# Kernel optimization log

Measured on AMD Instinct MI355X. Metric: run time of the kernel, lower is better.

## Reference

```python
import jax, jax.numpy as jnp
import numpy as np

K = 4          # conv kernel size
DIL = 3        # conv dilation
EPS = 1e-5     # rms eps inside gate kernel
NORM_EPS = 1e-5  # RMSNorm eps for value rms


def setup_inputs() -> dict:
    key = jax.random.key(0)
    ks = jax.random.split(key, 10)
    B, T, G, C, E = 2, 4096, 4, 1024, 1024
    return {
        "embeddings": jax.random.normal(ks[0], (B, T, E), jnp.float32),
        "hidden_states": jax.random.normal(ks[1], (B, T, G, C), jnp.float32),
        "key_w": jax.random.normal(ks[2], (G * C, E), jnp.float32) * 0.02,
        "key_b": jax.random.normal(ks[3], (G * C,), jnp.float32) * 0.02,
        "value_w": jax.random.normal(ks[4], (C, E), jnp.float32) * 0.02,
        "value_b": jax.random.normal(ks[5], (C,), jnp.float32) * 0.02,
        "w_key_norm": jax.random.uniform(ks[6], (G, C), jnp.float32, 0.5, 1.5),
        "w_query_norm": jax.random.uniform(ks[7], (G, C), jnp.float32, 0.5, 1.5),
        "w_norm": jax.random.uniform(ks[8], (G, C), jnp.float32, 0.5, 1.5),
        "conv_weight": jax.random.normal(ks[9], (G * C, K), jnp.float32) * 0.1,
    }


def reference(embeddings, hidden_states, key_w, key_b, value_w, value_b,
              w_key_norm, w_query_norm, w_norm, conv_weight):
    B, T, G, C = hidden_states.shape
    # projections
    k_all = (embeddings @ key_w.T + key_b).reshape(B, T, G, C)     # [B,T,G,C]
    q_all = hidden_states                                          # [B,T,G,C]
    vproj = embeddings @ value_w.T + value_b                       # [B,T,C]

    # gate kernel: per (b,t,g) RMS of key/query + weighted dot -> sign-sqrt-sigmoid gate
    rms_k = jnp.sqrt(jnp.mean(k_all * k_all, axis=-1) + EPS)       # [B,T,G]
    rms_q = jnp.sqrt(jnp.mean(q_all * q_all, axis=-1) + EPS)       # [B,T,G]
    dot = jnp.einsum('btgc,gc,btgc,gc->btg', k_all, w_key_norm, q_all, w_query_norm)
    gate_raw = dot / (rms_k * rms_q) / jnp.sqrt(jnp.float32(C))
    gate = jax.nn.sigmoid(jnp.where(gate_raw >= 0, 1.0, -1.0)
                          * jnp.sqrt(jnp.maximum(jnp.abs(gate_raw), 1e-6)))
    value = vproj[:, :, None, :] * gate[..., None]                 # [B,T,G,C]
    rms_v = jnp.sqrt(jnp.mean(value * value, axis=-1) + NORM_EPS)  # [B,T,G]

    # conv+residual kernel: per-group RMS-norm, dilated depthwise causal conv, SiLU, residual
    normed = value * (w_norm[None, None] / rms_v[..., None])       # [B,T,G,C]
    conv_w = conv_weight.reshape(G, C, K)                          # depthwise weights
    pad = (K - 1) * DIL
    xp = jnp.pad(normed, ((0, 0), (pad, 0), (0, 0), (0, 0)))
    # acc[b,t,g,c] = sum_k normed[b, t-(K-1-k)*DIL, g, c] * conv_w[g,c,k]
    acc = xp[:, 0:T] * conv_w[None, None, :, :, 0]
    for k in range(1, K):
        acc = acc + xp[:, k * DIL: k * DIL + T] * conv_w[None, None, :, :, k]
    acc = acc * jax.nn.sigmoid(acc)  # SiLU activation
    return value + acc
```

## Files before the change

### kernel.cpp

```cpp
#include <hip/hip_runtime.h>
#include <hip/hip_bf16.h>
#include <cstdint>
#include <cstddef>

using bf16 = __hip_bfloat16;

typedef __bf16 bf16x8_t __attribute__((ext_vector_type(8)));
typedef float  f32x4_t  __attribute__((ext_vector_type(4)));

static constexpr int Bb = 2;
static constexpr int Tt = 4096;
static constexpr int Gg = 4;
static constexpr int Cc = 1024;
static constexpr int Mm = Bb * Tt;
static constexpr int GC = Gg * Cc;

__device__ __forceinline__ float bfbits2f(unsigned u) {
  union { unsigned i; float f; } c; c.i = u << 16; return c.f;
}
__device__ __forceinline__ ushort f2bfbits(float v) {
  union { __hip_bfloat16 h; ushort u; } c; c.h = __float2bfloat16(v); return c.u;
}

__device__ __forceinline__ void store_val(bf16* p, float v)  { *p = __float2bfloat16(v); }
__device__ __forceinline__ void store_val(float* p, float v) { *p = v; }

__device__ __forceinline__ void gld_lds16(const ushort* g, ushort* l) {
  __builtin_amdgcn_global_load_lds(
      (const __attribute__((address_space(1))) void*)g,
      (__attribute__((address_space(3))) void*)l, 16, 0, 0);
}

__global__ __launch_bounds__(256)
void cvt_bf16(const float* __restrict__ in, ushort* __restrict__ out, int n4)
{
  const int i = blockIdx.x * 256 + threadIdx.x;
  if (i >= n4) return;
  const float4 v = ((const float4*)in)[i];
  ushort4 o;
  o.x = f2bfbits(v.x); o.y = f2bfbits(v.y);
  o.z = f2bfbits(v.z); o.w = f2bfbits(v.w);
  ((ushort4*)out)[i] = o;
}

__global__ __launch_bounds__(256)
void cvt_split(const float* __restrict__ in, ushort* __restrict__ hi,
               ushort* __restrict__ lo, int n4)
{
  const int i = blockIdx.x * 256 + threadIdx.x;
  if (i >= n4) return;
  const float4 v = ((const float4*)in)[i];
  ushort4 h, l;
  h.x = f2bfbits(v.x); l.x = f2bfbits(v.x - bfbits2f(h.x));
  h.y = f2bfbits(v.y); l.y = f2bfbits(v.y - bfbits2f(h.y));
  h.z = f2bfbits(v.z); l.z = f2bfbits(v.z - bfbits2f(h.z));
  h.w = f2bfbits(v.w); l.w = f2bfbits(v.w - bfbits2f(h.w));
  ((ushort4*)hi)[i] = h;
  ((ushort4*)lo)[i] = l;
}

__global__ __launch_bounds__(512, 1)
void gemm_key_fused(const ushort* __restrict__ embH, const ushort* __restrict__ embL,
                    const ushort* __restrict__ kwH,  const ushort* __restrict__ kwL,
                    const float* __restrict__ key_b, const float* __restrict__ hid,
                    const float* __restrict__ wkn,   const float* __restrict__ wqn,
                    float* __restrict__ k2_part, float* __restrict__ dot_part,
                    float* __restrict__ q2_part)
{
  constexpr int NT = 32;
  __shared__ __align__(16) ushort sA[2 * 16384];
  __shared__ __align__(16) ushort sB[2 * 16384];

  const int tid  = threadIdx.x;
  const int lane = tid & 63;
  const int wave = tid >> 6;
  const int wm   = wave & 1;
  const int wn   = wave >> 1;
  const int l15  = lane & 15;
  const int cHk  = (lane >> 4) ^ (lane & 7);
  const int row0 = blockIdx.y * 256;
  const int col0 = blockIdx.x * 256;

  const int sRow = tid >> 3;
  const int schk = (tid & 7) ^ (sRow & 7);
  const ushort* aSel = (schk < 4) ? embH : embL;
  const ushort* bSel = (schk < 4) ? kwH  : kwL;
  const int sel8 = (schk & 3) * 8;
  const int wofs = wave * 512;

  auto stageA = [&](int rb, int u, int b) {
    const size_t co = (size_t)u * 32 + sel8;
    gld_lds16(aSel + (size_t)(row0 + rb + sRow) * Cc + co,
              sA + b * 16384 + (rb >> 6) * 4096 + wofs);
    gld_lds16(aSel + (size_t)(row0 + rb + 64 + sRow) * Cc + co,
              sA + b * 16384 + ((rb >> 6) + 1) * 4096 + wofs);
  };
  auto stageB = [&](int rb, int u, int b) {
    const size_t co = (size_t)u * 32 + sel8;
    gld_lds16(bSel + (size_t)(col0 + rb + sRow) * Cc + co,
              sB + b * 16384 + (rb >> 6) * 4096 + wofs);
    gld_lds16(bSel + (size_t)(col0 + rb + 64 + sRow) * Cc + co,
              sB + b * 16384 + ((rb >> 6) + 1) * 4096 + wofs);
  };

  f32x4_t acc[2][2][4][2] = {};

#define MFMA3(QM, QN, AH, AL, BH, BL)                                       \
  _Pragma("unroll") for (int mi = 0; mi < 4; ++mi)                          \
    _Pragma("unroll") for (int ni = 0; ni < 2; ++ni) {                      \
      acc[QM][QN][mi][ni] = __builtin_amdgcn_mfma_f32_16x16x32_bf16(        \
          AH[mi], BH[ni], acc[QM][QN][mi][ni], 0, 0, 0);                    \
      acc[QM][QN][mi][ni] = __builtin_amdgcn_mfma_f32_16x16x32_bf16(        \
          AH[mi], BL[ni], acc[QM][QN][mi][ni], 0, 0, 0);                    \
      acc[QM][QN][mi][ni] = __builtin_amdgcn_mfma_f32_16x16x32_bf16(        \
          AL[mi], BH[ni], acc[QM][QN][mi][ni], 0, 0, 0);                    \
    }

  stageA(0, 0, 0); stageB(0, 0, 0); stageB(128, 0, 0); stageA(128, 0, 0);
  asm volatile("s_waitcnt vmcnt(0)" ::: "memory");
  __builtin_amdgcn_s_barrier();

  for (int u = 0; u < NT; ++u) {
    const int b = u & 1, nb = b ^ 1;
    const ushort* bufA = sA + b * 16384;
    const ushort* bufB = sB + b * 16384;
    if (u + 1 < NT) {
      stageA(0, u + 1, nb);   stageB(0, u + 1, nb);
      stageB(128, u + 1, nb); stageA(128, u + 1, nb);
    }

    bf16x8_t b0H[2], b0L[2], b1H[2], b1L[2];
#pragma unroll
    for (int ni = 0; ni < 2; ++ni) {
      const ushort* p0 = bufB + (wn * 32 + ni * 16 + l15) * 64;
      const ushort* p1 = bufB + (128 + wn * 32 + ni * 16 + l15) * 64;
      b0H[ni] = *(const bf16x8_t*)(p0 + cHk * 8);
      b0L[ni] = *(const bf16x8_t*)(p0 + (cHk ^ 4) * 8);
      b1H[ni] = *(const bf16x8_t*)(p1 + cHk * 8);
      b1L[ni] = *(const bf16x8_t*)(p1 + (cHk ^ 4) * 8);
    }
    bf16x8_t a0H[4], a0L[4];
#pragma unroll
    for (int mi = 0; mi < 4; ++mi) {
      const ushort* pa = bufA + (wm * 64 + mi * 16 + l15) * 64;
      a0H[mi] = *(const bf16x8_t*)(pa + cHk * 8);
      a0L[mi] = *(const bf16x8_t*)(pa + (cHk ^ 4) * 8);
    }
    __builtin_amdgcn_s_setprio(1);
    MFMA3(0, 0, a0H, a0L, b0H, b0L)
    __builtin_amdgcn_s_setprio(0);
    bf16x8_t a1H[4], a1L[4];
#pragma unroll
    for (int mi = 0; mi < 4; ++mi) {
      const ushort* pa = bufA + (128 + wm * 64 + mi * 16 + l15) * 64;
      a1H[mi] = *(const bf16x8_t*)(pa + cHk * 8);
      a1L[mi] = *(const bf16x8_t*)(pa + (cHk ^ 4) * 8);
    }
    __builtin_amdgcn_s_setprio(1);
    MFMA3(0, 1, a0H, a0L, b1H, b1L)
    MFMA3(1, 0, a1H, a1L, b0H, b0L)
    MFMA3(1, 1, a1H, a1L, b1H, b1L)
    __builtin_amdgcn_s_setprio(0);

    asm volatile("s_waitcnt lgkmcnt(0)" ::: "memory");
    asm volatile("s_waitcnt vmcnt(0)" ::: "memory");
    __builtin_amdgcn_s_barrier();
  }
#undef MFMA3

  const int lrow = lane >> 4;
  const int lcol = lane & 15;
  const int g    = col0 >> 10;

#pragma unroll
  for (int qm = 0; qm < 2; ++qm) {
    float s2[4][4] = {}, su[4][4] = {}, sq[4][4] = {};
#pragma unroll
    for (int qn = 0; qn < 2; ++qn)
#pragma unroll
      for (int ni = 0; ni < 2; ++ni) {
        const int col = col0 + qn * 128 + wn * 32 + ni * 16 + lcol;
        const float kb = key_b[col];
        const float ww = wkn[col] * wqn[col];
#pragma unroll
        for (int mi = 0; mi < 4; ++mi) {
          const int rowb = row0 + qm * 128 + wm * 64 + mi * 16 + lrow * 4;
#pragma unroll
          for (int r = 0; r < 4; ++r) {
            const float q = hid[(size_t)(rowb + r) * GC + col];
            const float k = acc[qm][qn][mi][ni][r] + kb;
            s2[mi][r] += k * k;
            su[mi][r] += k * ww * q;
            sq[mi][r] += q * q;
          }
        }
      }
#pragma unroll
    for (int off = 1; off < 16; off <<= 1) {
#pragma unroll
      for (int mi = 0; mi < 4; ++mi)
#pragma unroll
        for (int r = 0; r < 4; ++r) {
          s2[mi][r] += __shfl_xor(s2[mi][r], off);
          su[mi][r] += __shfl_xor(su[mi][r], off);
          sq[mi][r] += __shfl_xor(sq[mi][r], off);
        }
    }
    if (lcol == 0) {
#pragma unroll
      for (int mi = 0; mi < 4; ++mi) {
        const int rowb = row0 + qm * 128 + wm * 64 + mi * 16 + lrow * 4;
#pragma unroll
        for (int r = 0; r < 4; ++r) {
          atomicAdd(&k2_part[(rowb + r) * Gg + g],  s2[mi][r]);
          atomicAdd(&dot_part[(rowb + r) * Gg + g], su[mi][r]);
          atomicAdd(&q2_part[(rowb + r) * Gg + g],  sq[mi][r]);
        }
      }
    }
  }
}

template <typename OutT>
__global__ __launch_bounds__(256, 4)
void gemm_bt(const ushort* __restrict__ A, const ushort* __restrict__ Bm,
             const float* __restrict__ bias, OutT* __restrict__ C,
             int M, int N, int K)
{
  __shared__ __align__(16) ushort sA[128 * 64];
  __shared__ __align__(16) ushort sB[128 * 64];

  const int tid  = threadIdx.x;
  const int lane = tid & 63;
  const int wave = tid >> 6;
  const int wm   = wave & 1;
  const int wn   = wave >> 1;
  const int row0 = blockIdx.y * 128;
  const int col0 = blockIdx.x * 128;

  const int srow = tid >> 3;
  const int scol = ((tid & 7) ^ (srow & 7)) * 8;
  ushort* aWB = sA + wave * 512;
  ushort* bWB = sB + wave * 512;

  f32x4_t acc[4][4] = {};

  for (int kt = 0; kt < K; kt += 64) {
#pragma unroll
    for (int p = 0; p < 4; ++p) {
      gld_lds16(A  + (size_t)(row0 + p * 32 + srow) * K + kt + scol,
                aWB + p * 2048);
      gld_lds16(Bm + (size_t)(col0 + p * 32 + srow) * K + kt + scol,
                bWB + p * 2048);
    }
    __syncthreads();

#pragma unroll
    for (int ks = 0; ks < 2; ++ks) {
      const int cb = ks * 4 + (lane >> 4);
      const int ce = ((cb ^ (lane & 7)) * 8);
      bf16x8_t af[4], bfr[4];
#pragma unroll
      for (int mi = 0; mi < 4; ++mi) {
        const int r = wm * 64 + mi * 16 + (lane & 15);
        af[mi] = *(const bf16x8_t*)(sA + r * 64 + ce);
      }
#pragma unroll
      for (int ni = 0; ni < 4; ++ni) {
        const int r = wn * 64 + ni * 16 + (lane & 15);
        bfr[ni] = *(const bf16x8_t*)(sB + r * 64 + ce);
      }
#pragma unroll
      for (int mi = 0; mi < 4; ++mi)
#pragma unroll
        for (int ni = 0; ni < 4; ++ni)
          acc[mi][ni] = __builtin_amdgcn_mfma_f32_16x16x32_bf16(
              af[mi], bfr[ni], acc[mi][ni], 0, 0, 0);
    }
    __syncthreads();
  }

  const int lrow = lane >> 4;
  const int lcol = lane & 15;
#pragma unroll
  for (int ni = 0; ni < 4; ++ni) {
    const int col = col0 + wn * 64 + ni * 16 + lcol;
    const float bv = bias[col];
#pragma unroll
    for (int mi = 0; mi < 4; ++mi) {
      const int rowb = row0 + wm * 64 + mi * 16 + lrow * 4;
#pragma unroll
      for (int r = 0; r < 4; ++r)
        store_val(&C[(size_t)(rowb + r) * N + col], acc[mi][ni][r] + bv);
    }
  }
}

__global__ __launch_bounds__(256)
void finalize_kernel(const float* __restrict__ vproj,
                     const float* __restrict__ k2_part,
                     const float* __restrict__ dot_part,
                     const float* __restrict__ q2_part,
                     float* __restrict__ gate_o, float* __restrict__ snorm_o)
{
  const int bt   = blockIdx.x;
  const int tid  = threadIdx.x;
  const int g    = tid >> 6;
  const int lane = tid & 63;

  const float4 v4 = ((const float4*)(vproj + (size_t)bt * Cc))[tid];
  float pv = v4.x * v4.x + v4.y * v4.y + v4.z * v4.z + v4.w * v4.w;
#pragma unroll
  for (int off = 32; off > 0; off >>= 1) pv += __shfl_xor(pv, off);
  __shared__ float wsum[4];
  if (lane == 0) wsum[g] = pv;
  __syncthreads();

  if (lane == 0) {
    const float mv = (wsum[0] + wsum[1] + wsum[2] + wsum[3]) * (1.0f / 1024.0f);
    const float sk = k2_part[bt * Gg + g];
    const float sd = dot_part[bt * Gg + g];
    const float sq = q2_part[bt * Gg + g];
    const float rk = sqrtf(sk * (1.0f / 1024.0f) + 1e-5f);
    const float rq = sqrtf(sq * (1.0f / 1024.0f) + 1e-5f);
    const float graw = sd / (rk * rq) * (1.0f / 32.0f);
    const float sgn = (graw >= 0.f) ? 1.f : -1.f;
    const float gate = 1.f / (1.f + expf(-sgn * sqrtf(fmaxf(fabsf(graw), 1e-6f))));
    const float rv = sqrtf(gate * gate * mv + 1e-5f);
    gate_o[bt * Gg + g]  = gate;
    snorm_o[bt * Gg + g] = gate / rv;
  }
}

static constexpr int CJ  = 128;
static constexpr int NCH = 11;

__global__ __launch_bounds__(256)
void conv_kernel(const float* __restrict__ vproj, const float* __restrict__ gate,
                 const float* __restrict__ snorm, const float* __restrict__ wnm,
                 const float* __restrict__ cw, float* __restrict__ out)
{
  int x = blockIdx.x;
  const int cb = x & 3;  x >>= 2;
  const int p  = x % 3;  x /= 3;
  const int ch = x % NCH; x /= NCH;
  const int g  = x & 3;  x >>= 2;
  const int b  = x;
  const int c  = cb * 256 + threadIdx.x;

  const float wn = wnm[g * Cc + c];
  const float4 w = ((const float4*)cw)[g * Cc + c];

  int t = p + 3 * (ch * CJ);
  if (t >= Tt) return;

  float n1 = 0.f, n2 = 0.f, n3 = 0.f;
#pragma unroll
  for (int h = 3; h >= 1; --h) {
    const int th = t - 3 * h;
    float nv = 0.f;
    if (th >= 0) {
      const int bt = b * Tt + th;
      nv = vproj[(size_t)bt * Cc + c] * snorm[bt * Gg + g] * wn;
    }
    n3 = n2; n2 = n1; n1 = nv;
  }

  for (int j = 0; j < CJ && t < Tt; ++j, t += 3) {
    const int bt = b * Tt + t;
    const float vp  = vproj[(size_t)bt * Cc + c];
    const float gt  = gate[bt * Gg + g];
    const float sn  = snorm[bt * Gg + g];
    const float cur = vp * sn * wn;
    const float a   = w.x * n3 + w.y * n2 + w.z * n1 + w.w * cur;
    const float si  = a / (1.f + __expf(-a));
    out[((size_t)bt * Gg + g) * Cc + c] = vp * gt + si;
    n3 = n2; n2 = n1; n1 = cur;
  }
}

extern "C" void kernel_launch(void* const* d_in, const int* in_sizes, int n_in,
                              void* d_out, int out_size, void* d_ws, size_t ws_size,
                              hipStream_t stream)
{
  const float* emb   = (const float*)d_in[0];
  const float* hid   = (const float*)d_in[1];
  const float* key_w = (const float*)d_in[2];
  const float* key_b = (const float*)d_in[3];
  const float* val_w = (const float*)d_in[4];
  const float* val_b = (const float*)d_in[5];
  const float* wkn   = (const float*)d_in[6];
  const float* wqn   = (const float*)d_in[7];
  const float* wnm   = (const float*)d_in[8];
  const float* cwt   = (const float*)d_in[9];
  float* out = (float*)d_out;

  char* ws = (char*)d_ws;
  ushort* embH  = (ushort*)ws;  ws += (size_t)Mm * Cc * 2;
  ushort* embL  = (ushort*)ws;  ws += (size_t)Mm * Cc * 2;
  ushort* kwH   = (ushort*)ws;  ws += (size_t)GC * Cc * 2;
  ushort* kwL   = (ushort*)ws;  ws += (size_t)GC * Cc * 2;
  ushort* vwB   = (ushort*)ws;  ws += (size_t)Cc * Cc * 2;
  float*  vproj = (float*)ws;   ws += (size_t)Mm * Cc * 4;
  float*  k2p   = (float*)ws;   ws += (size_t)Mm * Gg * 4;
  float*  dotp  = (float*)ws;   ws += (size_t)Mm * Gg * 4;
  float*  q2p   = (float*)ws;   ws += (size_t)Mm * Gg * 4;
  float*  gate  = (float*)ws;   ws += (size_t)Mm * Gg * 4;
  float*  snorm = (float*)ws;

  hipMemsetAsync(k2p, 0, (size_t)3 * Mm * Gg * 4, stream);

  dim3 blk(256);
  cvt_split<<<dim3((Mm * Cc / 4) / 256), blk, 0, stream>>>(emb,   embH, embL, Mm * Cc / 4);
  cvt_split<<<dim3((GC * Cc / 4) / 256), blk, 0, stream>>>(key_w, kwH,  kwL,  GC * Cc / 4);
  cvt_bf16 <<<dim3((Cc * Cc / 4) / 256), blk, 0, stream>>>(val_w, vwB,  Cc * Cc / 4);

  gemm_key_fused<<<dim3(GC / 256, Mm / 256), dim3(512), 0, stream>>>(
      embH, embL, kwH, kwL, key_b, hid, wkn, wqn, k2p, dotp, q2p);

  gemm_bt<float><<<dim3(Cc / 128, Mm / 128), blk, 0, stream>>>(
      embH, vwB, val_b, vproj, Mm, Cc, Cc);

  finalize_kernel<<<dim3(Mm), blk, 0, stream>>>(vproj, k2p, dotp, q2p, gate, snorm);

  const int nblocks = Bb * Gg * NCH * 3 * (Cc / 256);
  conv_kernel<<<dim3(nblocks), blk, 0, stream>>>(vproj, gate, snorm, wnm, cwt, out);
}
```

Before: 584.9 us.

## Fuse conversions and memset, move value RMS into GEMM epilogue, drop finalize kernel

The two fp32-to-bf16 split conversions, the plain bf16 conversion and the zeroing of the partial-sum buffers become one launch that dispatches on block index. The value-projection GEMM epilogue now accumulates per-row sums of squares into a new buffer with atomics. The finalize kernel is removed: the conv kernel computes gate and norm scale inline from the partial sums. The conv kernel is also vectorised to float4 per thread over four channels, with shorter time chunks. This removes a full extra read of vproj and several launches, at the cost of recomputing the gate scalar for every block that touches a row, and more atomics in the GEMM epilogue.

Measured after the change: 580.1 us. About the same (-0.8%).

```diff
diff --git a/kernel.cpp b/kernel.cpp
--- a/kernel.cpp
+++ b/kernel.cpp
@@ -22,9 +22,6 @@
   union { __hip_bfloat16 h; ushort u; } c; c.h = __float2bfloat16(v); return c.u;
 }
 
-__device__ __forceinline__ void store_val(bf16* p, float v)  { *p = __float2bfloat16(v); }
-__device__ __forceinline__ void store_val(float* p, float v) { *p = v; }
-
 __device__ __forceinline__ void gld_lds16(const ushort* g, ushort* l) {
   __builtin_amdgcn_global_load_lds(
       (const __attribute__((address_space(1))) void*)g,
@@ -32,31 +29,36 @@
 }
 
 __global__ __launch_bounds__(256)
-void cvt_bf16(const float* __restrict__ in, ushort* __restrict__ out, int n4)
-{
-  const int i = blockIdx.x * 256 + threadIdx.x;
-  if (i >= n4) return;
-  const float4 v = ((const float4*)in)[i];
-  ushort4 o;
-  o.x = f2bfbits(v.x); o.y = f2bfbits(v.y);
-  o.z = f2bfbits(v.z); o.w = f2bfbits(v.w);
-  ((ushort4*)out)[i] = o;
-}
-
-__global__ __launch_bounds__(256)
-void cvt_split(const float* __restrict__ in, ushort* __restrict__ hi,
-               ushort* __restrict__ lo, int n4)
-{
-  const int i = blockIdx.x * 256 + threadIdx.x;
-  if (i >= n4) return;
-  const float4 v = ((const float4*)in)[i];
-  ushort4 h, l;
-  h.x = f2bfbits(v.x); l.x = f2bfbits(v.x - bfbits2f(h.x));
-  h.y = f2bfbits(v.y); l.y = f2bfbits(v.y - bfbits2f(h.y));
-  h.z = f2bfbits(v.z); l.z = f2bfbits(v.z - bfbits2f(h.z));
-  h.w = f2bfbits(v.w); l.w = f2bfbits(v.w - bfbits2f(h.w));
-  ((ushort4*)hi)[i] = h;
-  ((ushort4*)lo)[i] = l;
+void cvt_all(const float* __restrict__ emb, const float* __restrict__ key_w,
+             const float* __restrict__ val_w,
+             ushort* __restrict__ embH, ushort* __restrict__ embL,
+             ushort* __restrict__ kwH,  ushort* __restrict__ kwL,
+             ushort* __restrict__ vwB,  float* __restrict__ zbase)
+{
+  const int bid = blockIdx.x;
+  const int tid = threadIdx.x;
+  if (bid < 12288) {
+    const bool isE = bid < 8192;
+    const int  i   = (isE ? bid : bid - 8192) * 256 + tid;
+    const float4 v = ((const float4*)(isE ? emb : key_w))[i];
+    ushort4 h, l;
+    h.x = f2bfbits(v.x); l.x = f2bfbits(v.x - bfbits2f(h.x));
+    h.y = f2bfbits(v.y); l.y = f2bfbits(v.y - bfbits2f(h.y));
+    h.z = f2bfbits(v.z); l.z = f2bfbits(v.z - bfbits2f(h.z));
+    h.w = f2bfbits(v.w); l.w = f2bfbits(v.w - bfbits2f(h.w));
+    ((ushort4*)(isE ? embH : kwH))[i] = h;
+    ((ushort4*)(isE ? embL : kwL))[i] = l;
+  } else if (bid < 13312) {
+    const int i = (bid - 12288) * 256 + tid;
+    const float4 v = ((const float4*)val_w)[i];
+    ushort4 o;
+    o.x = f2bfbits(v.x); o.y = f2bfbits(v.y);
+    o.z = f2bfbits(v.z); o.w = f2bfbits(v.w);
+    ((ushort4*)vwB)[i] = o;
+  } else {
+    const int i = (bid - 13312) * 256 + tid;
+    ((float4*)zbase)[i] = make_float4(0.f, 0.f, 0.f, 0.f);
+  }
 }
 
 __global__ __launch_bounds__(512, 1)
@@ -221,11 +223,10 @@
   }
 }
 
-template <typename OutT>
 __global__ __launch_bounds__(256, 4)
 void gemm_bt(const ushort* __restrict__ A, const ushort* __restrict__ Bm,
-             const float* __restrict__ bias, OutT* __restrict__ C,
-             int M, int N, int K)
+             const float* __restrict__ bias, float* __restrict__ C,
+             float* __restrict__ v2_part, int M, int N, int K)
 {
   __shared__ __align__(16) ushort sA[128 * 64];
   __shared__ __align__(16) ushort sB[128 * 64];
@@ -282,6 +283,7 @@
 
   const int lrow = lane >> 4;
   const int lcol = lane & 15;
+  float sv[4][4] = {};
 #pragma unroll
   for (int ni = 0; ni < 4; ++ni) {
     const int col = col0 + wn * 64 + ni * 16 + lcol;
@@ -290,91 +292,110 @@
     for (int mi = 0; mi < 4; ++mi) {
       const int rowb = row0 + wm * 64 + mi * 16 + lrow * 4;
 #pragma unroll
+      for (int r = 0; r < 4; ++r) {
+        const float v = acc[mi][ni][r] + bv;
+        C[(size_t)(rowb + r) * N + col] = v;
+        sv[mi][r] += v * v;
+      }
+    }
+  }
+#pragma unroll
+  for (int off = 1; off < 16; off <<= 1)
+#pragma unroll
+    for (int mi = 0; mi < 4; ++mi)
+#pragma unroll
       for (int r = 0; r < 4; ++r)
-        store_val(&C[(size_t)(rowb + r) * N + col], acc[mi][ni][r] + bv);
-    }
-  }
+        sv[mi][r] += __shfl_xor(sv[mi][r], off);
+  if (lcol == 0) {
+#pragma unroll
+    for (int mi = 0; mi < 4; ++mi) {
+      const int rowb = row0 + wm * 64 + mi * 16 + lrow * 4;
+#pragma unroll
+      for (int r = 0; r < 4; ++r)
+        atomicAdd(&v2_part[rowb + r], sv[mi][r]);
+    }
+  }
+}
+
+static constexpr int CJ2  = 32;
+static constexpr int NCH2 = 43;
+
+__device__ __forceinline__ float2 gate_snorm(
+    const float* __restrict__ k2p, const float* __restrict__ dotp,
+    const float* __restrict__ q2p, const float* __restrict__ v2p,
+    int bt, int g)
+{
+  const float sk = k2p[bt * Gg + g];
+  const float sd = dotp[bt * Gg + g];
+  const float sq = q2p[bt * Gg + g];
+  const float mv = v2p[bt] * (1.0f / 1024.0f);
+  const float rk = sqrtf(sk * (1.0f / 1024.0f) + 1e-5f);
+  const float rq = sqrtf(sq * (1.0f / 1024.0f) + 1e-5f);
+  const float graw = sd / (rk * rq) * (1.0f / 32.0f);
+  const float sgn = (graw >= 0.f) ? 1.f : -1.f;
+  const float gate = 1.f / (1.f + expf(-sgn * sqrtf(fmaxf(fabsf(graw), 1e-6f))));
+  const float rv = sqrtf(gate * gate * mv + 1e-5f);
+  return make_float2(gate, gate / rv);
 }
 
 __global__ __launch_bounds__(256)
-void finalize_kernel(const float* __restrict__ vproj,
-                     const float* __restrict__ k2_part,
-                     const float* __restrict__ dot_part,
-                     const float* __restrict__ q2_part,
-                     float* __restrict__ gate_o, float* __restrict__ snorm_o)
-{
-  const int bt   = blockIdx.x;
-  const int tid  = threadIdx.x;
-  const int g    = tid >> 6;
-  const int lane = tid & 63;
-
-  const float4 v4 = ((const float4*)(vproj + (size_t)bt * Cc))[tid];
-  float pv = v4.x * v4.x + v4.y * v4.y + v4.z * v4.z + v4.w * v4.w;
-#pragma unroll
-  for (int off = 32; off > 0; off >>= 1) pv += __shfl_xor(pv, off);
-  __shared__ float wsum[4];
-  if (lane == 0) wsum[g] = pv;
-  __syncthreads();
-
-  if (lane == 0) {
-    const float mv = (wsum[0] + wsum[1] + wsum[2] + wsum[3]) * (1.0f / 1024.0f);
-    const float sk = k2_part[bt * Gg + g];
-    const float sd = dot_part[bt * Gg + g];
-    const float sq = q2_part[bt * Gg + g];
-    const float rk = sqrtf(sk * (1.0f / 1024.0f) + 1e-5f);
-    const float rq = sqrtf(sq * (1.0f / 1024.0f) + 1e-5f);
-    const float graw = sd / (rk * rq) * (1.0f / 32.0f);
-    const float sgn = (graw >= 0.f) ? 1.f : -1.f;
-    const float gate = 1.f / (1.f + expf(-sgn * sqrtf(fmaxf(fabsf(graw), 1e-6f))));
-    const float rv = sqrtf(gate * gate * mv + 1e-5f);
-    gate_o[bt * Gg + g]  = gate;
-    snorm_o[bt * Gg + g] = gate / rv;
-  }
-}
-
-static constexpr int CJ  = 128;
-static constexpr int NCH = 11;
-
-__global__ __launch_bounds__(256)
-void conv_kernel(const float* __restrict__ vproj, const float* __restrict__ gate,
-                 const float* __restrict__ snorm, const float* __restrict__ wnm,
-                 const float* __restrict__ cw, float* __restrict__ out)
+void conv_kernel(const float* __restrict__ vproj,
+                 const float* __restrict__ k2p, const float* __restrict__ dotp,
+                 const float* __restrict__ q2p, const float* __restrict__ v2p,
+                 const float* __restrict__ wnm, const float* __restrict__ cw,
+                 float* __restrict__ out)
 {
   int x = blockIdx.x;
-  const int cb = x & 3;  x >>= 2;
-  const int p  = x % 3;  x /= 3;
-  const int ch = x % NCH; x /= NCH;
-  const int g  = x & 3;  x >>= 2;
+  const int p  = x % 3;    x /= 3;
+  const int ch = x % NCH2; x /= NCH2;
+  const int g  = x & 3;    x >>= 2;
   const int b  = x;
-  const int c  = cb * 256 + threadIdx.x;
-
-  const float wn = wnm[g * Cc + c];
-  const float4 w = ((const float4*)cw)[g * Cc + c];
-
-  int t = p + 3 * (ch * CJ);
+  const int c4 = threadIdx.x;
+
+  const float4 wn4 = ((const float4*)wnm)[g * 256 + c4];
+  const int cbase = g * Cc + 4 * c4;
+  const float4 w0 = ((const float4*)cw)[cbase + 0];
+  const float4 w1 = ((const float4*)cw)[cbase + 1];
+  const float4 w2 = ((const float4*)cw)[cbase + 2];
+  const float4 w3 = ((const float4*)cw)[cbase + 3];
+
+  int t = p + 3 * (ch * CJ2);
   if (t >= Tt) return;
 
-  float n1 = 0.f, n2 = 0.f, n3 = 0.f;
+  float4 n1 = make_float4(0,0,0,0), n2 = n1, n3 = n1;
 #pragma unroll
   for (int h = 3; h >= 1; --h) {
     const int th = t - 3 * h;
-    float nv = 0.f;
+    float4 nv = make_float4(0,0,0,0);
     if (th >= 0) {
       const int bt = b * Tt + th;
-      nv = vproj[(size_t)bt * Cc + c] * snorm[bt * Gg + g] * wn;
+      const float2 gs = gate_snorm(k2p, dotp, q2p, v2p, bt, g);
+      const float4 vp = ((const float4*)vproj)[(size_t)bt * 256 + c4];
+      const float s = gs.y;
+      nv = make_float4(vp.x * s * wn4.x, vp.y * s * wn4.y,
+                       vp.z * s * wn4.z, vp.w * s * wn4.w);
     }
     n3 = n2; n2 = n1; n1 = nv;
   }
 
-  for (int j = 0; j < CJ && t < Tt; ++j, t += 3) {
+  for (int j = 0; j < CJ2 && t < Tt; ++j, t += 3) {
     const int bt = b * Tt + t;
-    const float vp  = vproj[(size_t)bt * Cc + c];
-    const float gt  = gate[bt * Gg + g];
-    const float sn  = snorm[bt * Gg + g];
-    const float cur = vp * sn * wn;
-    const float a   = w.x * n3 + w.y * n2 + w.z * n1 + w.w * cur;
-    const float si  = a / (1.f + __expf(-a));
-    out[((size_t)bt * Gg + g) * Cc + c] = vp * gt + si;
+    const float2 gs = gate_snorm(k2p, dotp, q2p, v2p, bt, g);
+    const float4 vp = ((const float4*)vproj)[(size_t)bt * 256 + c4];
+    const float sn = gs.y, gt = gs.x;
+    float4 cur = make_float4(vp.x * sn * wn4.x, vp.y * sn * wn4.y,
+                             vp.z * sn * wn4.z, vp.w * sn * wn4.w);
+    float4 a;
+    a.x = w0.x * n3.x + w0.y * n2.x + w0.z * n1.x + w0.w * cur.x;
+    a.y = w1.x * n3.y + w1.y * n2.y + w1.z * n1.y + w1.w * cur.y;
+    a.z = w2.x * n3.z + w2.y * n2.z + w2.z * n1.z + w2.w * cur.z;
+    a.w = w3.x * n3.w + w3.y * n2.w + w3.z * n1.w + w3.w * cur.w;
+    float4 o;
+    o.x = vp.x * gt + a.x / (1.f + __expf(-a.x));
+    o.y = vp.y * gt + a.y / (1.f + __expf(-a.y));
+    o.z = vp.z * gt + a.z / (1.f + __expf(-a.z));
+    o.w = vp.w * gt + a.w / (1.f + __expf(-a.w));
+    ((float4*)out)[((size_t)bt * Gg + g) * 256 + c4] = o;
     n3 = n2; n2 = n1; n1 = cur;
   }
 }
@@ -405,24 +426,18 @@
   float*  k2p   = (float*)ws;   ws += (size_t)Mm * Gg * 4;
   float*  dotp  = (float*)ws;   ws += (size_t)Mm * Gg * 4;
   float*  q2p   = (float*)ws;   ws += (size_t)Mm * Gg * 4;
-  float*  gate  = (float*)ws;   ws += (size_t)Mm * Gg * 4;
-  float*  snorm = (float*)ws;
-
-  hipMemsetAsync(k2p, 0, (size_t)3 * Mm * Gg * 4, stream);
-
-  dim3 blk(256);
-  cvt_split<<<dim3((Mm * Cc / 4) / 256), blk, 0, stream>>>(emb,   embH, embL, Mm * Cc / 4);
-  cvt_split<<<dim3((GC * Cc / 4) / 256), blk, 0, stream>>>(key_w, kwH,  kwL,  GC * Cc / 4);
-  cvt_bf16 <<<dim3((Cc * Cc / 4) / 256), blk, 0, stream>>>(val_w, vwB,  Cc * Cc / 4);
+  float*  v2p   = (float*)ws;
+
+  cvt_all<<<dim3(13416), dim3(256), 0, stream>>>(
+      emb, key_w, val_w, embH, embL, kwH, kwL, vwB, k2p);
 
   gemm_key_fused<<<dim3(GC / 256, Mm / 256), dim3(512), 0, stream>>>(
       embH, embL, kwH, kwL, key_b, hid, wkn, wqn, k2p, dotp, q2p);
 
-  gemm_bt<float><<<dim3(Cc / 128, Mm / 128), blk, 0, stream>>>(
-      embH, vwB, val_b, vproj, Mm, Cc, Cc);
-
-  finalize_kernel<<<dim3(Mm), blk, 0, stream>>>(vproj, k2p, dotp, q2p, gate, snorm);
-
-  const int nblocks = Bb * Gg * NCH * 3 * (Cc / 256);
-  conv_kernel<<<dim3(nblocks), blk, 0, stream>>>(vproj, gate, snorm, wnm, cwt, out);
-}
+  gemm_bt<<<dim3(Cc / 128, Mm / 128), dim3(256), 0, stream>>>(
+      embH, vwB, val_b, vproj, v2p, Mm, Cc, Cc);
+
+  const int nblocks = Bb * Gg * NCH2 * 3;
+  conv_kernel<<<dim3(nblocks), dim3(256), 0, stream>>>(
+      vproj, k2p, dotp, q2p, v2p, wnm, cwt, out);
+}
```
